# Performance work log

Measured on AMD Instinct MI355X. Metric: run time of the kernel, lower is better.

Reference implementation:

```python
import jax, jax.numpy as jnp
import numpy as np

B, N, H, O = 2, 512, 128, 32  # batch, n_particles, hidden_dim, obs_dim


def _linear_init(key, out_d, in_d):
    kw, kb = jax.random.split(key)
    s = 1.0 / np.sqrt(in_d)
    W = jax.random.uniform(kw, (out_d, in_d), minval=-s, maxval=s, dtype=jnp.float32)
    b = jax.random.uniform(kb, (out_d,), minval=-s, maxval=s, dtype=jnp.float32)
    return W, b


def setup_inputs() -> dict:
    key = jax.random.key(0)
    ks = jax.random.split(key, 8)
    z = jax.random.normal(ks[0], (B, N, H), dtype=jnp.float32)
    s_t = jax.random.normal(ks[1], (B, N, O), dtype=jnp.float32)
    W1, b1 = _linear_init(ks[2], H, 2 * H)   # relation_mlp layer 0
    W2, b2 = _linear_init(ks[3], H, H)       # relation_mlp layer 2
    Wq, bq = _linear_init(ks[4], H, H)       # query_proj
    Wk, bk = _linear_init(ks[5], H, O)       # key_proj
    W3, b3 = _linear_init(ks[6], H, H)       # aggregation_mlp layer 0
    W4, b4 = _linear_init(ks[7], H, H)       # aggregation_mlp layer 2
    return dict(z=z, s_t=s_t, W1=W1, b1=b1, W2=W2, b2=b2, Wq=Wq, bq=bq,
                Wk=Wk, bk=bk, W3=W3, b3=b3, W4=W4, b4=b4)


def reference(z, s_t, W1, b1, W2, b2, Wq, bq, Wk, bk, W3, b3, W4, b4):
    b_, n, h = z.shape
    # query depends only on i, key only on j (repeat in the original is redundant)
    q = z @ Wq.T + bq            # [B,N,H]
    k = s_t @ Wk.T + bk          # [B,N,H]
    scores = jnp.einsum('bih,bjh->bij', q, k) / (h ** 0.5)   # [B,N,N]
    eye = jnp.eye(n, dtype=bool)
    scores = jnp.where(eye, -jnp.inf, scores)
    attn = jax.nn.softmax(scores, axis=-1)                   # [B,N,N]
    # relation_mlp on concat(z_i, z_j): split first weight into i- and j- halves
    W1i, W1j = W1[:, :h], W1[:, h:]
    zi = z @ W1i.T               # [B,N,H]
    zj = z @ W1j.T               # [B,N,H]
    rel = jnp.tanh(zi[:, :, None, :] + zj[:, None, :, :] + b1) @ W2.T + b2  # [B,N,N,H]
    agg = jnp.einsum('bij,bijh->bih', attn, rel)             # weighted sum over j
    dz_dt = jnp.tanh(agg @ W3.T + b3) @ W4.T + b4
    return dz_dt
```

## Files before the change

### kernel.cpp

```cpp
#include <hip/hip_runtime.h>
#include <hip/hip_bf16.h>

#define NN 512
#define HH 128
#define OO 32

#define KL 2.8853900817779268f

__device__ __forceinline__ float vexp2(float x) {
    float r; asm("v_exp_f32 %0, %1" : "=v"(r) : "v"(x)); return r;
}
__device__ __forceinline__ float vrcp(float x) {
    float r; asm("v_rcp_f32 %0, %1" : "=v"(r) : "v"(x)); return r;
}
__device__ __forceinline__ float tanh_fast(float x) {
    float e = vexp2(KL * x);
    return 1.0f - 2.0f * vrcp(e + 1.0f);
}
__device__ __forceinline__ float waveRedMax(float v) {
#pragma unroll
    for (int off = 32; off > 0; off >>= 1) v = fmaxf(v, __shfl_xor(v, off, 64));
    return v;
}
__device__ __forceinline__ float waveRedSum(float v) {
#pragma unroll
    for (int off = 32; off > 0; off >>= 1) v += __shfl_xor(v, off, 64);
    return v;
}
__device__ __forceinline__ float red8(float v) {
    v += __shfl_xor(v, 1, 64); v += __shfl_xor(v, 2, 64); v += __shfl_xor(v, 4, 64);
    return v;
}
__device__ __forceinline__ float dot16r(const float4* w, const float* x, int rot) {
    float a = 0;
#pragma unroll
    for (int ii = 0; ii < 4; ii++) {
        int i = (ii + rot) & 3;
        float4 xv = *(const float4*)(x + i * 4);
        a = fmaf(xv.x, w[ii].x, a); a = fmaf(xv.y, w[ii].y, a);
        a = fmaf(xv.z, w[ii].z, a); a = fmaf(xv.w, w[ii].w, a);
    }
    return a;
}
__device__ __forceinline__ unsigned short f2bf(float x) {
    unsigned u = __float_as_uint(x);
    u += 0x7fffu + ((u >> 16) & 1u);
    return (unsigned short)(u >> 16);
}
__device__ __forceinline__ float bf_lo(unsigned u) { return __uint_as_float((u & 0xffffu) << 16); }
__device__ __forceinline__ float bf_hi(unsigned u) { return __uint_as_float(u & 0xffff0000u); }

__global__ __launch_bounds__(1024, 4) void ezj_kt_kernel(
    const float* __restrict__ z, const float* __restrict__ s_t,
    const float* __restrict__ W1, const float* __restrict__ Wk,
    const float* __restrict__ bk,
    unsigned short* __restrict__ EzjG, float* __restrict__ kTG) {
    __shared__ float zrow[4][HH];
    __shared__ float srow[4][OO];
    int t = threadIdx.x, bid = blockIdx.x;
    int r0 = bid * 4;
    int b = bid >> 7, i0 = (bid & 127) * 4;
    if (t < 4 * HH) zrow[t >> 7][t & 127] = z[(size_t)r0 * HH + t];
    else if (t < 4 * HH + 4 * OO) {
        int u = t - 4 * HH;
        srow[u >> 5][u & 31] = s_t[(size_t)r0 * OO + u];
    }
    __syncthreads();

    int kq = t & 7, h = t >> 3, rot = (kq >> 1) & 3;
    {
        const float4* Wp = (const float4*)(W1 + (size_t)h * 2 * HH + HH) + kq * 4;
        float4 w[4];
#pragma unroll
        for (int ii = 0; ii < 4; ii++) w[ii] = Wp[(ii + rot) & 3];
        float a0 = red8(dot16r(w, &zrow[0][kq * 16], rot));
        float a1 = red8(dot16r(w, &zrow[1][kq * 16], rot));
        float a2 = red8(dot16r(w, &zrow[2][kq * 16], rot));
        float a3 = red8(dot16r(w, &zrow[3][kq * 16], rot));
        if (kq == 0) {
            EzjG[(size_t)(r0 + 0) * HH + h] = f2bf(vexp2(KL * a0));
            EzjG[(size_t)(r0 + 1) * HH + h] = f2bf(vexp2(KL * a1));
            EzjG[(size_t)(r0 + 2) * HH + h] = f2bf(vexp2(KL * a2));
            EzjG[(size_t)(r0 + 3) * HH + h] = f2bf(vexp2(KL * a3));
        }
    }
    {
        float4 wk = ((const float4*)(Wk + (size_t)h * OO))[kq];
        float4 s0 = *(const float4*)&srow[0][kq * 4];
        float4 s1 = *(const float4*)&srow[1][kq * 4];
        float4 s2 = *(const float4*)&srow[2][kq * 4];
        float4 s3 = *(const float4*)&srow[3][kq * 4];
        float a0 = red8(s0.x * wk.x + s0.y * wk.y + s0.z * wk.z + s0.w * wk.w);
        float a1 = red8(s1.x * wk.x + s1.y * wk.y + s1.z * wk.z + s1.w * wk.w);
        float a2 = red8(s2.x * wk.x + s2.y * wk.y + s2.z * wk.z + s2.w * wk.w);
        float a3 = red8(s3.x * wk.x + s3.y * wk.y + s3.z * wk.z + s3.w * wk.w);
        if (kq == 0) {
            float vbk = bk[h];
            float4 kv = make_float4(a0 + vbk, a1 + vbk, a2 + vbk, a3 + vbk);
            *(float4*)(kTG + ((size_t)b * HH + h) * NN + i0) = kv;
        }
    }
}

__global__ __launch_bounds__(1024, 4) void fused_kernel(
    const float* __restrict__ z,
    const float* __restrict__ Wq, const float* __restrict__ bq,
    const float* __restrict__ W1, const float* __restrict__ b1,
    const float* __restrict__ kTG, const unsigned short* __restrict__ EzjG,
    const float* __restrict__ W2, const float* __restrict__ b2,
    const float* __restrict__ W3, const float* __restrict__ b3,
    const float* __restrict__ W4, const float* __restrict__ b4,
    float* __restrict__ out) {
    __shared__ float zrow[4][HH];
    __shared__ float q4T[HH][4];
    __shared__ float c4T[HH][4];
    __shared__ float attnT[NN][4];
    __shared__ float buf[8192];
    __shared__ float UL[4][HH];
    __shared__ float aggL[4][HH];
    __shared__ float h1L[4][HH];
    __shared__ float redA[16], redB[16];

    float (*scp)[4][NN] = (float (*)[4][NN])buf;
    float (*part)[4][HH] = (float (*)[4][HH])buf;

    int t = threadIdx.x;
    int bid = blockIdx.x;
    int b = bid >> 7;
    int i0 = (bid & 127) * 4;
    int r0 = bid * 4;

    if (t < 4 * HH) zrow[t >> 7][t & 127] = z[(size_t)r0 * HH + t];
    __syncthreads();

    {
        int kq = t & 7, h = t >> 3, rot = (kq >> 1) & 3;
        float4 w[4];
        {
            const float4* Wp = (const float4*)(Wq + (size_t)h * HH) + kq * 4;
#pragma unroll
            for (int ii = 0; ii < 4; ii++) w[ii] = Wp[(ii + rot) & 3];
            float a0 = red8(dot16r(w, &zrow[0][kq * 16], rot));
            float a1 = red8(dot16r(w, &zrow[1][kq * 16], rot));
            float a2 = red8(dot16r(w, &zrow[2][kq * 16], rot));
            float a3 = red8(dot16r(w, &zrow[3][kq * 16], rot));
            if (kq == 0) {
                float vbq = bq[h];
                q4T[h][0] = a0 + vbq; q4T[h][1] = a1 + vbq;
                q4T[h][2] = a2 + vbq; q4T[h][3] = a3 + vbq;
            }
        }
        {
            const float4* Wp = (const float4*)(W1 + (size_t)h * 2 * HH) + kq * 4;
#pragma unroll
            for (int ii = 0; ii < 4; ii++) w[ii] = Wp[(ii + rot) & 3];
            float a0 = red8(dot16r(w, &zrow[0][kq * 16], rot));
            float a1 = red8(dot16r(w, &zrow[1][kq * 16], rot));
            float a2 = red8(dot16r(w, &zrow[2][kq * 16], rot));
            float a3 = red8(dot16r(w, &zrow[3][kq * 16], rot));
            if (kq == 0) {
                float vb1 = b1[h];
                c4T[h][0] = vexp2(KL * (a0 + vb1)); c4T[h][1] = vexp2(KL * (a1 + vb1));
                c4T[h][2] = vexp2(KL * (a2 + vb1)); c4T[h][3] = vexp2(KL * (a3 + vb1));
            }
        }
    }
    __syncthreads();

    {
        int j = t & 511, hs = t >> 9, h0 = hs * 64;
        const float* kb = kTG + ((size_t)b * HH + h0) * NN + j;
        float s0 = 0, s1 = 0, s2 = 0, s3 = 0;
#pragma unroll 8
        for (int hh = 0; hh < 64; hh++) {
            float kv = kb[(size_t)hh * NN];
            float4 qv = *(const float4*)q4T[h0 + hh];
            s0 = fmaf(qv.x, kv, s0); s1 = fmaf(qv.y, kv, s1);
            s2 = fmaf(qv.z, kv, s2); s3 = fmaf(qv.w, kv, s3);
        }
        scp[hs][0][j] = s0; scp[hs][1][j] = s1;
        scp[hs][2][j] = s2; scp[hs][3][j] = s3;
    }
    __syncthreads();

    {
        int rp = t >> 9, j = t & 511;
        int lr0 = rp * 2, lr1 = lr0 + 1;
        const float sc = 0.08838834764831845f;
        float s0 = (scp[0][lr0][j] + scp[1][lr0][j]) * sc;
        float s1 = (scp[0][lr1][j] + scp[1][lr1][j]) * sc;
        if (j == i0 + lr0) s0 = -1e30f;
        if (j == i0 + lr1) s1 = -1e30f;
        int lane = t & 63, w = t >> 6, wb = rp * 8;
        float m0 = waveRedMax(s0), m1 = waveRedMax(s1);
        if (lane == 0) { redA[w] = m0; redB[w] = m1; }
        __syncthreads();
        float mm0 = redA[wb], mm1 = redB[wb];
#pragma unroll
        for (int k = 1; k < 8; k++) { mm0 = fmaxf(mm0, redA[wb + k]); mm1 = fmaxf(mm1, redB[wb + k]); }
        float e0 = __expf(s0 - mm0), e1 = __expf(s1 - mm1);
        float p0 = waveRedSum(e0), p1 = waveRedSum(e1);
        __syncthreads();
        if (lane == 0) { redA[w] = p0; redB[w] = p1; }
        __syncthreads();
        float S0 = redA[wb], S1 = redB[wb];
#pragma unroll
        for (int k = 1; k < 8; k++) { S0 += redA[wb + k]; S1 += redB[wb + k]; }
        attnT[j][lr0] = e0 * __fdividef(1.0f, S0);
        attnT[j][lr1] = e1 * __fdividef(1.0f, S1);
    }
    __syncthreads();

    {
        int lane6 = t & 63, qs = t >> 6;
        int hp = lane6 * 2;
        float4 cA = *(const float4*)c4T[hp];
        float4 cB = *(const float4*)c4T[hp + 1];
        const unsigned* zbU = (const unsigned*)(EzjG + (size_t)b * NN * HH) + lane6;
        float a0A = 0, a1A = 0, a2A = 0, a3A = 0;
        float a0B = 0, a1B = 0, a2B = 0, a3B = 0;
        int jb = qs * 32;
#pragma unroll 8
        for (int jj = 0; jj < 32; jj++) {
            int j = jb + jj;
            unsigned u = zbU[(size_t)j * 64];
            float Ex = bf_lo(u), Ey = bf_hi(u);
            float4 w = *(const float4*)attnT[j];
            a0A = fmaf(w.x, vrcp(fmaf(cA.x, Ex, 1.0f)), a0A);
            a1A = fmaf(w.y, vrcp(fmaf(cA.y, Ex, 1.0f)), a1A);
            a2A = fmaf(w.z, vrcp(fmaf(cA.z, Ex, 1.0f)), a2A);
            a3A = fmaf(w.w, vrcp(fmaf(cA.w, Ex, 1.0f)), a3A);
            a0B = fmaf(w.x, vrcp(fmaf(cB.x, Ey, 1.0f)), a0B);
            a1B = fmaf(w.y, vrcp(fmaf(cB.y, Ey, 1.0f)), a1B);
            a2B = fmaf(w.z, vrcp(fmaf(cB.z, Ey, 1.0f)), a2B);
            a3B = fmaf(w.w, vrcp(fmaf(cB.w, Ey, 1.0f)), a3B);
        }
        __syncthreads();
        *(float2*)&part[qs][0][hp] = make_float2(a0A, a0B);
        *(float2*)&part[qs][1][hp] = make_float2(a1A, a1B);
        *(float2*)&part[qs][2][hp] = make_float2(a2A, a2B);
        *(float2*)&part[qs][3][hp] = make_float2(a3A, a3B);
    }
    __syncthreads();
    if (t < 512) {
        int r = t >> 7, h = t & 127;
        float s = 0;
#pragma unroll
        for (int q = 0; q < 16; q++) s += part[q][r][h];
        UL[r][h] = fmaf(-2.0f, s, 1.0f);
    }
    __syncthreads();

    {
        int kq = t & 7, h = t >> 3, rot = (kq >> 1) & 3;
        float4 w[4];
        {
            const float4* Wp = (const float4*)(W2 + (size_t)h * HH) + kq * 4;
#pragma unroll
            for (int ii = 0; ii < 4; ii++) w[ii] = Wp[(ii + rot) & 3];
            float a0 = red8(dot16r(w, &UL[0][kq * 16], rot));
            float a1 = red8(dot16r(w, &UL[1][kq * 16], rot));
            float a2 = red8(dot16r(w, &UL[2][kq * 16], rot));
            float a3 = red8(dot16r(w, &UL[3][kq * 16], rot));
            if (kq == 0) {
                float vb2 = b2[h];
                aggL[0][h] = a0 + vb2; aggL[1][h] = a1 + vb2;
                aggL[2][h] = a2 + vb2; aggL[3][h] = a3 + vb2;
            }
        }
        __syncthreads();
        {
            const float4* Wp = (const float4*)(W3 + (size_t)h * HH) + kq * 4;
#pragma unroll
            for (int ii = 0; ii < 4; ii++) w[ii] = Wp[(ii + rot) & 3];
            float a0 = red8(dot16r(w, &aggL[0][kq * 16], rot));
            float a1 = red8(dot16r(w, &aggL[1][kq * 16], rot));
            float a2 = red8(dot16r(w, &aggL[2][kq * 16], rot));
            float a3 = red8(dot16r(w, &aggL[3][kq * 16], rot));
            if (kq == 0) {
                float vb3 = b3[h];
                h1L[0][h] = tanh_fast(a0 + vb3); h1L[1][h] = tanh_fast(a1 + vb3);
                h1L[2][h] = tanh_fast(a2 + vb3); h1L[3][h] = tanh_fast(a3 + vb3);
            }
        }
        __syncthreads();
        {
            const float4* Wp = (const float4*)(W4 + (size_t)h * HH) + kq * 4;
#pragma unroll
            for (int ii = 0; ii < 4; ii++) w[ii] = Wp[(ii + rot) & 3];
            float a0 = red8(dot16r(w, &h1L[0][kq * 16], rot));
            float a1 = red8(dot16r(w, &h1L[1][kq * 16], rot));
            float a2 = red8(dot16r(w, &h1L[2][kq * 16], rot));
            float a3 = red8(dot16r(w, &h1L[3][kq * 16], rot));
            if (kq == 0) {
                float vb4 = b4[h];
                out[(size_t)(r0 + 0) * HH + h] = a0 + vb4;
                out[(size_t)(r0 + 1) * HH + h] = a1 + vb4;
                out[(size_t)(r0 + 2) * HH + h] = a2 + vb4;
                out[(size_t)(r0 + 3) * HH + h] = a3 + vb4;
            }
        }
    }
}

extern "C" void kernel_launch(void* const* d_in, const int* in_sizes, int n_in,
                              void* d_out, int out_size, void* d_ws, size_t ws_size,
                              hipStream_t stream) {
    const float* z   = (const float*)d_in[0];
    const float* s_t = (const float*)d_in[1];
    const float* W1  = (const float*)d_in[2];
    const float* b1  = (const float*)d_in[3];
    const float* W2  = (const float*)d_in[4];
    const float* b2  = (const float*)d_in[5];
    const float* Wq  = (const float*)d_in[6];
    const float* bq  = (const float*)d_in[7];
    const float* Wk  = (const float*)d_in[8];
    const float* bk  = (const float*)d_in[9];
    const float* W3  = (const float*)d_in[10];
    const float* b3  = (const float*)d_in[11];
    const float* W4  = (const float*)d_in[12];
    const float* b4  = (const float*)d_in[13];
    float* out = (float*)d_out;

    float* ws = (float*)d_ws;
    float* kT = ws;
    unsigned short* Ezj = (unsigned short*)(ws + 131072);

    hipLaunchKernelGGL(ezj_kt_kernel, dim3(256), dim3(1024), 0, stream,
                       z, s_t, W1, Wk, bk, Ezj, kT);
    hipLaunchKernelGGL(fused_kernel, dim3(256), dim3(1024), 0, stream,
                       z, Wq, bq, W1, b1, kT, Ezj, W2, b2, W3, b3, W4, b4, out);
}
```

Baseline: 35.94 us.

## Move q/c projections into prep kernel and prefetch global loads before barriers

The query and i-half relation projections move from the fused kernel into the prep kernel, which writes them to workspace for the fused kernel to load. In the fused kernel, kT columns and Ezj rows are prefetched into registers before the barriers so their latency overlaps shared-memory work. W2/W3/W4 weights and biases are loaded before the reduction barrier, and a separate pair of reduction arrays removes one barrier from the softmax. This raises register pressure (64+ live values) and adds workspace traffic for qP/cP.

```diff
diff --git a/kernel.cpp b/kernel.cpp
--- a/kernel.cpp
+++ b/kernel.cpp
@@ -50,16 +50,32 @@
 __device__ __forceinline__ float bf_lo(unsigned u) { return __uint_as_float((u & 0xffffu) << 16); }
 __device__ __forceinline__ float bf_hi(unsigned u) { return __uint_as_float(u & 0xffff0000u); }
 
-__global__ __launch_bounds__(1024, 4) void ezj_kt_kernel(
+__global__ __launch_bounds__(1024, 4) void prep_kernel(
     const float* __restrict__ z, const float* __restrict__ s_t,
-    const float* __restrict__ W1, const float* __restrict__ Wk,
-    const float* __restrict__ bk,
+    const float* __restrict__ W1, const float* __restrict__ b1,
+    const float* __restrict__ Wq, const float* __restrict__ bq,
+    const float* __restrict__ Wk, const float* __restrict__ bk,
+    float* __restrict__ qP, float* __restrict__ cP,
     unsigned short* __restrict__ EzjG, float* __restrict__ kTG) {
     __shared__ float zrow[4][HH];
     __shared__ float srow[4][OO];
     int t = threadIdx.x, bid = blockIdx.x;
-    int r0 = bid * 4;
-    int b = bid >> 7, i0 = (bid & 127) * 4;
+    int r0 = bid * 4, b = bid >> 7, i0 = (bid & 127) * 4;
+    int kq = t & 7, h = t >> 3, rot = (kq >> 1) & 3;
+
+    const float4* WqP = (const float4*)(Wq + (size_t)h * HH) + kq * 4;
+    const float4* WiP = (const float4*)(W1 + (size_t)h * 2 * HH) + kq * 4;
+    const float4* WjP = (const float4*)(W1 + (size_t)h * 2 * HH + HH) + kq * 4;
+    float4 wq[4], wi[4], wj[4];
+#pragma unroll
+    for (int ii = 0; ii < 4; ii++) {
+        wq[ii] = WqP[(ii + rot) & 3];
+        wi[ii] = WiP[(ii + rot) & 3];
+        wj[ii] = WjP[(ii + rot) & 3];
+    }
+    float4 wk = ((const float4*)(Wk + (size_t)h * OO))[kq];
+    float vbq = bq[h], vb1 = b1[h], vbk = bk[h];
+
     if (t < 4 * HH) zrow[t >> 7][t & 127] = z[(size_t)r0 * HH + t];
     else if (t < 4 * HH + 4 * OO) {
         int u = t - 4 * HH;
@@ -67,16 +83,32 @@
     }
     __syncthreads();
 
-    int kq = t & 7, h = t >> 3, rot = (kq >> 1) & 3;
-    {
-        const float4* Wp = (const float4*)(W1 + (size_t)h * 2 * HH + HH) + kq * 4;
-        float4 w[4];
-#pragma unroll
-        for (int ii = 0; ii < 4; ii++) w[ii] = Wp[(ii + rot) & 3];
-        float a0 = red8(dot16r(w, &zrow[0][kq * 16], rot));
-        float a1 = red8(dot16r(w, &zrow[1][kq * 16], rot));
-        float a2 = red8(dot16r(w, &zrow[2][kq * 16], rot));
-        float a3 = red8(dot16r(w, &zrow[3][kq * 16], rot));
+    {
+        float a0 = red8(dot16r(wq, &zrow[0][kq * 16], rot));
+        float a1 = red8(dot16r(wq, &zrow[1][kq * 16], rot));
+        float a2 = red8(dot16r(wq, &zrow[2][kq * 16], rot));
+        float a3 = red8(dot16r(wq, &zrow[3][kq * 16], rot));
+        if (kq == 0) {
+            float* qp = qP + (size_t)bid * 512 + h * 4;
+            qp[0] = a0 + vbq; qp[1] = a1 + vbq; qp[2] = a2 + vbq; qp[3] = a3 + vbq;
+        }
+    }
+    {
+        float a0 = red8(dot16r(wi, &zrow[0][kq * 16], rot));
+        float a1 = red8(dot16r(wi, &zrow[1][kq * 16], rot));
+        float a2 = red8(dot16r(wi, &zrow[2][kq * 16], rot));
+        float a3 = red8(dot16r(wi, &zrow[3][kq * 16], rot));
+        if (kq == 0) {
+            float* cp = cP + (size_t)bid * 512 + h * 4;
+            cp[0] = vexp2(KL * (a0 + vb1)); cp[1] = vexp2(KL * (a1 + vb1));
+            cp[2] = vexp2(KL * (a2 + vb1)); cp[3] = vexp2(KL * (a3 + vb1));
+        }
+    }
+    {
+        float a0 = red8(dot16r(wj, &zrow[0][kq * 16], rot));
+        float a1 = red8(dot16r(wj, &zrow[1][kq * 16], rot));
+        float a2 = red8(dot16r(wj, &zrow[2][kq * 16], rot));
+        float a3 = red8(dot16r(wj, &zrow[3][kq * 16], rot));
         if (kq == 0) {
             EzjG[(size_t)(r0 + 0) * HH + h] = f2bf(vexp2(KL * a0));
             EzjG[(size_t)(r0 + 1) * HH + h] = f2bf(vexp2(KL * a1));
@@ -85,7 +117,6 @@
         }
     }
     {
-        float4 wk = ((const float4*)(Wk + (size_t)h * OO))[kq];
         float4 s0 = *(const float4*)&srow[0][kq * 4];
         float4 s1 = *(const float4*)&srow[1][kq * 4];
         float4 s2 = *(const float4*)&srow[2][kq * 4];
@@ -95,7 +126,6 @@
         float a2 = red8(s2.x * wk.x + s2.y * wk.y + s2.z * wk.z + s2.w * wk.w);
         float a3 = red8(s3.x * wk.x + s3.y * wk.y + s3.z * wk.z + s3.w * wk.w);
         if (kq == 0) {
-            float vbk = bk[h];
             float4 kv = make_float4(a0 + vbk, a1 + vbk, a2 + vbk, a3 + vbk);
             *(float4*)(kTG + ((size_t)b * HH + h) * NN + i0) = kv;
         }
@@ -103,15 +133,12 @@
 }
 
 __global__ __launch_bounds__(1024, 4) void fused_kernel(
-    const float* __restrict__ z,
-    const float* __restrict__ Wq, const float* __restrict__ bq,
-    const float* __restrict__ W1, const float* __restrict__ b1,
+    const float* __restrict__ qP, const float* __restrict__ cP,
     const float* __restrict__ kTG, const unsigned short* __restrict__ EzjG,
     const float* __restrict__ W2, const float* __restrict__ b2,
     const float* __restrict__ W3, const float* __restrict__ b3,
     const float* __restrict__ W4, const float* __restrict__ b4,
     float* __restrict__ out) {
-    __shared__ float zrow[4][HH];
     __shared__ float q4T[HH][4];
     __shared__ float c4T[HH][4];
     __shared__ float attnT[NN][4];
@@ -119,113 +146,86 @@
     __shared__ float UL[4][HH];
     __shared__ float aggL[4][HH];
     __shared__ float h1L[4][HH];
-    __shared__ float redA[16], redB[16];
+    __shared__ float redA[16], redB[16], redC[16], redD[16];
 
     float (*scp)[4][NN] = (float (*)[4][NN])buf;
     float (*part)[4][HH] = (float (*)[4][HH])buf;
 
-    int t = threadIdx.x;
-    int bid = blockIdx.x;
-    int b = bid >> 7;
-    int i0 = (bid & 127) * 4;
-    int r0 = bid * 4;
-
-    if (t < 4 * HH) zrow[t >> 7][t & 127] = z[(size_t)r0 * HH + t];
-    __syncthreads();
-
-    {
-        int kq = t & 7, h = t >> 3, rot = (kq >> 1) & 3;
-        float4 w[4];
-        {
-            const float4* Wp = (const float4*)(Wq + (size_t)h * HH) + kq * 4;
-#pragma unroll
-            for (int ii = 0; ii < 4; ii++) w[ii] = Wp[(ii + rot) & 3];
-            float a0 = red8(dot16r(w, &zrow[0][kq * 16], rot));
-            float a1 = red8(dot16r(w, &zrow[1][kq * 16], rot));
-            float a2 = red8(dot16r(w, &zrow[2][kq * 16], rot));
-            float a3 = red8(dot16r(w, &zrow[3][kq * 16], rot));
-            if (kq == 0) {
-                float vbq = bq[h];
-                q4T[h][0] = a0 + vbq; q4T[h][1] = a1 + vbq;
-                q4T[h][2] = a2 + vbq; q4T[h][3] = a3 + vbq;
-            }
-        }
-        {
-            const float4* Wp = (const float4*)(W1 + (size_t)h * 2 * HH) + kq * 4;
-#pragma unroll
-            for (int ii = 0; ii < 4; ii++) w[ii] = Wp[(ii + rot) & 3];
-            float a0 = red8(dot16r(w, &zrow[0][kq * 16], rot));
-            float a1 = red8(dot16r(w, &zrow[1][kq * 16], rot));
-            float a2 = red8(dot16r(w, &zrow[2][kq * 16], rot));
-            float a3 = red8(dot16r(w, &zrow[3][kq * 16], rot));
-            if (kq == 0) {
-                float vb1 = b1[h];
-                c4T[h][0] = vexp2(KL * (a0 + vb1)); c4T[h][1] = vexp2(KL * (a1 + vb1));
-                c4T[h][2] = vexp2(KL * (a2 + vb1)); c4T[h][3] = vexp2(KL * (a3 + vb1));
-            }
-        }
-    }
-    __syncthreads();
-
-    {
-        int j = t & 511, hs = t >> 9, h0 = hs * 64;
-        const float* kb = kTG + ((size_t)b * HH + h0) * NN + j;
-        float s0 = 0, s1 = 0, s2 = 0, s3 = 0;
-#pragma unroll 8
-        for (int hh = 0; hh < 64; hh++) {
-            float kv = kb[(size_t)hh * NN];
-            float4 qv = *(const float4*)q4T[h0 + hh];
-            s0 = fmaf(qv.x, kv, s0); s1 = fmaf(qv.y, kv, s1);
-            s2 = fmaf(qv.z, kv, s2); s3 = fmaf(qv.w, kv, s3);
-        }
-        scp[hs][0][j] = s0; scp[hs][1][j] = s1;
-        scp[hs][2][j] = s2; scp[hs][3][j] = s3;
-    }
-    __syncthreads();
-
-    {
-        int rp = t >> 9, j = t & 511;
+    int t = threadIdx.x, bid = blockIdx.x;
+    int b = bid >> 7, i0 = (bid & 127) * 4, r0 = bid * 4;
+
+    if (t < 512) ((float*)q4T)[t] = qP[(size_t)bid * 512 + t];
+    else         ((float*)c4T)[t - 512] = cP[(size_t)bid * 512 + (t - 512)];
+
+    int j = t & 511, hs = t >> 9, h0 = hs * 64;
+    const float* kb = kTG + ((size_t)b * HH + h0) * NN + j;
+    float kv[32];
+#pragma unroll
+    for (int hh = 0; hh < 32; hh++) kv[hh] = kb[(size_t)hh * NN];
+    __syncthreads();
+
+    float s0 = 0, s1 = 0, s2 = 0, s3 = 0;
+#pragma unroll
+    for (int hh = 0; hh < 32; hh++) {
+        float4 qv = *(const float4*)q4T[h0 + hh];
+        s0 = fmaf(qv.x, kv[hh], s0); s1 = fmaf(qv.y, kv[hh], s1);
+        s2 = fmaf(qv.z, kv[hh], s2); s3 = fmaf(qv.w, kv[hh], s3);
+    }
+#pragma unroll
+    for (int hh = 0; hh < 32; hh++) kv[hh] = kb[(size_t)(32 + hh) * NN];
+#pragma unroll
+    for (int hh = 0; hh < 32; hh++) {
+        float4 qv = *(const float4*)q4T[h0 + 32 + hh];
+        s0 = fmaf(qv.x, kv[hh], s0); s1 = fmaf(qv.y, kv[hh], s1);
+        s2 = fmaf(qv.z, kv[hh], s2); s3 = fmaf(qv.w, kv[hh], s3);
+    }
+    scp[hs][0][j] = s0; scp[hs][1][j] = s1;
+    scp[hs][2][j] = s2; scp[hs][3][j] = s3;
+
+    int lane6 = t & 63, qs = t >> 6, hp = lane6 * 2, jb = qs * 32;
+    const unsigned* zbU = (const unsigned*)EzjG + (size_t)b * NN * (HH / 2) + lane6;
+    unsigned uv[32];
+#pragma unroll
+    for (int jj = 0; jj < 32; jj++) uv[jj] = zbU[(size_t)(jb + jj) * (HH / 2)];
+    __syncthreads();
+
+    {
+        int rp = t >> 9;
         int lr0 = rp * 2, lr1 = lr0 + 1;
         const float sc = 0.08838834764831845f;
-        float s0 = (scp[0][lr0][j] + scp[1][lr0][j]) * sc;
-        float s1 = (scp[0][lr1][j] + scp[1][lr1][j]) * sc;
-        if (j == i0 + lr0) s0 = -1e30f;
-        if (j == i0 + lr1) s1 = -1e30f;
+        float c0 = (scp[0][lr0][j] + scp[1][lr0][j]) * sc;
+        float c1 = (scp[0][lr1][j] + scp[1][lr1][j]) * sc;
+        if (j == i0 + lr0) c0 = -1e30f;
+        if (j == i0 + lr1) c1 = -1e30f;
         int lane = t & 63, w = t >> 6, wb = rp * 8;
-        float m0 = waveRedMax(s0), m1 = waveRedMax(s1);
+        float m0 = waveRedMax(c0), m1 = waveRedMax(c1);
         if (lane == 0) { redA[w] = m0; redB[w] = m1; }
         __syncthreads();
         float mm0 = redA[wb], mm1 = redB[wb];
 #pragma unroll
         for (int k = 1; k < 8; k++) { mm0 = fmaxf(mm0, redA[wb + k]); mm1 = fmaxf(mm1, redB[wb + k]); }
-        float e0 = __expf(s0 - mm0), e1 = __expf(s1 - mm1);
+        float e0 = __expf(c0 - mm0), e1 = __expf(c1 - mm1);
         float p0 = waveRedSum(e0), p1 = waveRedSum(e1);
+        if (lane == 0) { redC[w] = p0; redD[w] = p1; }
         __syncthreads();
-        if (lane == 0) { redA[w] = p0; redB[w] = p1; }
-        __syncthreads();
-        float S0 = redA[wb], S1 = redB[wb];
-#pragma unroll
-        for (int k = 1; k < 8; k++) { S0 += redA[wb + k]; S1 += redB[wb + k]; }
+        float S0 = redC[wb], S1 = redD[wb];
+#pragma unroll
+        for (int k = 1; k < 8; k++) { S0 += redC[wb + k]; S1 += redD[wb + k]; }
         attnT[j][lr0] = e0 * __fdividef(1.0f, S0);
         attnT[j][lr1] = e1 * __fdividef(1.0f, S1);
     }
     __syncthreads();
 
     {
-        int lane6 = t & 63, qs = t >> 6;
-        int hp = lane6 * 2;
         float4 cA = *(const float4*)c4T[hp];
         float4 cB = *(const float4*)c4T[hp + 1];
-        const unsigned* zbU = (const unsigned*)(EzjG + (size_t)b * NN * HH) + lane6;
         float a0A = 0, a1A = 0, a2A = 0, a3A = 0;
         float a0B = 0, a1B = 0, a2B = 0, a3B = 0;
-        int jb = qs * 32;
-#pragma unroll 8
+#pragma unroll
         for (int jj = 0; jj < 32; jj++) {
-            int j = jb + jj;
-            unsigned u = zbU[(size_t)j * 64];
-            float Ex = bf_lo(u), Ey = bf_hi(u);
-            float4 w = *(const float4*)attnT[j];
+            int jc = jb + jj;
+            float Ex = bf_lo(uv[jj]), Ey = bf_hi(uv[jj]);
+            float4 w = *(const float4*)attnT[jc];
             a0A = fmaf(w.x, vrcp(fmaf(cA.x, Ex, 1.0f)), a0A);
             a1A = fmaf(w.y, vrcp(fmaf(cA.y, Ex, 1.0f)), a1A);
             a2A = fmaf(w.z, vrcp(fmaf(cA.z, Ex, 1.0f)), a2A);
@@ -235,13 +235,26 @@
             a2B = fmaf(w.z, vrcp(fmaf(cB.z, Ey, 1.0f)), a2B);
             a3B = fmaf(w.w, vrcp(fmaf(cB.w, Ey, 1.0f)), a3B);
         }
-        __syncthreads();
         *(float2*)&part[qs][0][hp] = make_float2(a0A, a0B);
         *(float2*)&part[qs][1][hp] = make_float2(a1A, a1B);
         *(float2*)&part[qs][2][hp] = make_float2(a2A, a2B);
         *(float2*)&part[qs][3][hp] = make_float2(a3A, a3B);
     }
-    __syncthreads();
+
+    int kq = t & 7, h8 = t >> 3, rot = (kq >> 1) & 3;
+    const float4* W2p = (const float4*)(W2 + (size_t)h8 * HH) + kq * 4;
+    const float4* W3p = (const float4*)(W3 + (size_t)h8 * HH) + kq * 4;
+    const float4* W4p = (const float4*)(W4 + (size_t)h8 * HH) + kq * 4;
+    float4 w2[4], w3[4], w4[4];
+#pragma unroll
+    for (int ii = 0; ii < 4; ii++) {
+        w2[ii] = W2p[(ii + rot) & 3];
+        w3[ii] = W3p[(ii + rot) & 3];
+        w4[ii] = W4p[(ii + rot) & 3];
+    }
+    float vb2 = b2[h8], vb3 = b3[h8], vb4 = b4[h8];
+    __syncthreads();
+
     if (t < 512) {
         int r = t >> 7, h = t & 127;
         float s = 0;
@@ -252,53 +265,37 @@
     __syncthreads();
 
     {
-        int kq = t & 7, h = t >> 3, rot = (kq >> 1) & 3;
-        float4 w[4];
-        {
-            const float4* Wp = (const float4*)(W2 + (size_t)h * HH) + kq * 4;
-#pragma unroll
-            for (int ii = 0; ii < 4; ii++) w[ii] = Wp[(ii + rot) & 3];
-            float a0 = red8(dot16r(w, &UL[0][kq * 16], rot));
-            float a1 = red8(dot16r(w, &UL[1][kq * 16], rot));
-            float a2 = red8(dot16r(w, &UL[2][kq * 16], rot));
-            float a3 = red8(dot16r(w, &UL[3][kq * 16], rot));
-            if (kq == 0) {
-                float vb2 = b2[h];
-                aggL[0][h] = a0 + vb2; aggL[1][h] = a1 + vb2;
-                aggL[2][h] = a2 + vb2; aggL[3][h] = a3 + vb2;
-            }
-        }
-        __syncthreads();
-        {
-            const float4* Wp = (const float4*)(W3 + (size_t)h * HH) + kq * 4;
-#pragma unroll
-            for (int ii = 0; ii < 4; ii++) w[ii] = Wp[(ii + rot) & 3];
-            float a0 = red8(dot16r(w, &aggL[0][kq * 16], rot));
-            float a1 = red8(dot16r(w, &aggL[1][kq * 16], rot));
-            float a2 = red8(dot16r(w, &aggL[2][kq * 16], rot));
-            float a3 = red8(dot16r(w, &aggL[3][kq * 16], rot));
-            if (kq == 0) {
-                float vb3 = b3[h];
-                h1L[0][h] = tanh_fast(a0 + vb3); h1L[1][h] = tanh_fast(a1 + vb3);
-                h1L[2][h] = tanh_fast(a2 + vb3); h1L[3][h] = tanh_fast(a3 + vb3);
-            }
-        }
-        __syncthreads();
-        {
-            const float4* Wp = (const float4*)(W4 + (size_t)h * HH) + kq * 4;
-#pragma unroll
-            for (int ii = 0; ii < 4; ii++) w[ii] = Wp[(ii + rot) & 3];
-            float a0 = red8(dot16r(w, &h1L[0][kq * 16], rot));
-            float a1 = red8(dot16r(w, &h1L[1][kq * 16], rot));
-            float a2 = red8(dot16r(w, &h1L[2][kq * 16], rot));
-            float a3 = red8(dot16r(w, &h1L[3][kq * 16], rot));
-            if (kq == 0) {
-                float vb4 = b4[h];
-                out[(size_t)(r0 + 0) * HH + h] = a0 + vb4;
-                out[(size_t)(r0 + 1) * HH + h] = a1 + vb4;
-                out[(size_t)(r0 + 2) * HH + h] = a2 + vb4;
-                out[(size_t)(r0 + 3) * HH + h] = a3 + vb4;
-            }
+        float a0 = red8(dot16r(w2, &UL[0][kq * 16], rot));
+        float a1 = red8(dot16r(w2, &UL[1][kq * 16], rot));
+        float a2 = red8(dot16r(w2, &UL[2][kq * 16], rot));
+        float a3 = red8(dot16r(w2, &UL[3][kq * 16], rot));
+        if (kq == 0) {
+            aggL[0][h8] = a0 + vb2; aggL[1][h8] = a1 + vb2;
+            aggL[2][h8] = a2 + vb2; aggL[3][h8] = a3 + vb2;
+        }
+    }
+    __syncthreads();
+    {
+        float a0 = red8(dot16r(w3, &aggL[0][kq * 16], rot));
+        float a1 = red8(dot16r(w3, &aggL[1][kq * 16], rot));
+        float a2 = red8(dot16r(w3, &aggL[2][kq * 16], rot));
+        float a3 = red8(dot16r(w3, &aggL[3][kq * 16], rot));
+        if (kq == 0) {
+            h1L[0][h8] = tanh_fast(a0 + vb3); h1L[1][h8] = tanh_fast(a1 + vb3);
+            h1L[2][h8] = tanh_fast(a2 + vb3); h1L[3][h8] = tanh_fast(a3 + vb3);
+        }
+    }
+    __syncthreads();
+    {
+        float a0 = red8(dot16r(w4, &h1L[0][kq * 16], rot));
+        float a1 = red8(dot16r(w4, &h1L[1][kq * 16], rot));
+        float a2 = red8(dot16r(w4, &h1L[2][kq * 16], rot));
+        float a3 = red8(dot16r(w4, &h1L[3][kq * 16], rot));
+        if (kq == 0) {
+            out[(size_t)(r0 + 0) * HH + h8] = a0 + vb4;
+            out[(size_t)(r0 + 1) * HH + h8] = a1 + vb4;
+            out[(size_t)(r0 + 2) * HH + h8] = a2 + vb4;
+            out[(size_t)(r0 + 3) * HH + h8] = a3 + vb4;
         }
     }
 }
@@ -324,10 +321,12 @@
 
     float* ws = (float*)d_ws;
     float* kT = ws;
-    unsigned short* Ezj = (unsigned short*)(ws + 131072);
-
-    hipLaunchKernelGGL(ezj_kt_kernel, dim3(256), dim3(1024), 0, stream,
-                       z, s_t, W1, Wk, bk, Ezj, kT);
+    float* qP = ws + 131072;
+    float* cP = ws + 262144;
+    unsigned short* Ezj = (unsigned short*)(ws + 393216);
+
+    hipLaunchKernelGGL(prep_kernel, dim3(256), dim3(1024), 0, stream,
+                       z, s_t, W1, b1, Wq, bq, Wk, bk, qP, cP, Ezj, kT);
     hipLaunchKernelGGL(fused_kernel, dim3(256), dim3(1024), 0, stream,
-                       z, Wq, bq, W1, b1, kT, Ezj, W2, b2, W3, b3, W4, b4, out);
-}
+                       qP, cP, kT, Ezj, W2, b2, W3, b3, W4, b4, out);
+}
```

New measurement: 35.51 us. No clear change (-1.2%).
